# Performance work log

Measured on AMD Instinct MI355X. Metric: run time of the kernel, lower is better.

The kernel has to match this reference:

```python
import jax, jax.numpy as jnp
import numpy as np

N_NODES = 30000
N_EDGES = 240000
N_GRAPHS = 300
IN_CH = 5


def _bn(x, p):
    # inference batchnorm; p = stack([gamma, beta, running_mean, running_var]), shape (4, C)
    g, b, m, v = p
    return g * (x - m) * jax.lax.rsqrt(v + 1e-5) + b


def _gatv2(x, src, dst, wl, bl, wr, br, att, bias, heads, outc, concat):
    # PyG GATv2Conv: e_ij = att . leaky_relu(lin_l(x_j) + lin_r(x_i)), softmax over edges into i,
    # out_i = sum_j alpha_ij * lin_l(x_j)
    n = x.shape[0]
    xl = (x @ wl + bl).reshape(n, heads, outc)  # source-side transform
    xr = (x @ wr + br).reshape(n, heads, outc)  # target-side transform
    e = jax.nn.leaky_relu(xl[src] + xr[dst], 0.2)          # [E, H, C]
    logit = jnp.einsum('ehc,hc->eh', e, att)               # [E, H]
    lmax = jax.ops.segment_max(logit, dst, num_segments=n)
    lmax = jnp.where(jnp.isfinite(lmax), lmax, 0.0)        # empty segments -> 0
    ex = jnp.exp(logit - lmax[dst])
    den = jax.ops.segment_sum(ex, dst, num_segments=n)
    alpha = ex / (den[dst] + 1e-16)                        # PyG softmax eps
    out = jax.ops.segment_sum(xl[src] * alpha[..., None], dst, num_segments=n)
    out = out.reshape(n, heads * outc) if concat else out.mean(axis=1)
    return out + bias


def _forward(x, edge_index, batch, w_in, b_in, bn_in,
             g1_wl, g1_bl, g1_wr, g1_br, g1_att, g1_bias, bn1,
             g2_wl, g2_bl, g2_wr, g2_br, g2_att, g2_bias, bn2,
             g3_wl, g3_bl, g3_wr, g3_br, g3_att, g3_bias, bn3,
             c_w1, c_b1, c_bn, c_w2, c_b2, c_w3, c_b3):
    n = x.shape[0]
    loops = jnp.arange(n)
    src = jnp.concatenate([edge_index[0], loops])  # add_self_loops=True
    dst = jnp.concatenate([edge_index[1], loops])
    h = jax.nn.relu(_bn(x @ w_in + b_in, bn_in))
    h = jax.nn.elu(_bn(_gatv2(h, src, dst, g1_wl, g1_bl, g1_wr, g1_br, g1_att, g1_bias, 4, 64, True), bn1))
    h = jax.nn.elu(_bn(_gatv2(h, src, dst, g2_wl, g2_bl, g2_wr, g2_br, g2_att, g2_bias, 4, 64, True), bn2))
    h = jax.nn.elu(_bn(_gatv2(h, src, dst, g3_wl, g3_bl, g3_wr, g3_br, g3_att, g3_bias, 1, 128, False), bn3))
    cnt = jax.ops.segment_sum(jnp.ones((n,), h.dtype), batch, num_segments=N_GRAPHS)
    mean = jax.ops.segment_sum(h, batch, num_segments=N_GRAPHS) / jnp.maximum(cnt, 1.0)[:, None]
    mx = jax.ops.segment_max(h, batch, num_segments=N_GRAPHS)
    mx = jnp.where(jnp.isfinite(mx), mx, 0.0)
    g = jnp.concatenate([mean, mx], axis=1)                # (B, 256)
    z = jax.nn.relu(_bn(g @ c_w1 + c_b1, c_bn))
    z = jax.nn.relu(z @ c_w2 + c_b2)
    return jax.nn.log_softmax(z @ c_w3 + c_b3, axis=-1)    # (B, 2)


def setup_inputs() -> dict:
    base = jax.random.key(0)
    k = lambda i: jax.random.fold_in(base, i)
    def lin(i, fi, fo):
        return jax.random.normal(k(i), (fi, fo), jnp.float32) / np.sqrt(np.float32(fi))
    def vec(i, c):
        return jax.random.normal(k(i), (c,), jnp.float32) * 0.05
    def bn(i, c):
        g = jax.random.uniform(k(i), (c,), jnp.float32) + 0.5
        b = jax.random.normal(jax.random.fold_in(k(i), 1), (c,), jnp.float32) * 0.1
        return jnp.stack([g, b, jnp.zeros((c,), jnp.float32), jnp.ones((c,), jnp.float32)])
    def att(i, h, c):
        return jax.random.normal(k(i), (h, c), jnp.float32) / np.sqrt(np.float32(c))
    return dict(
        x=jax.random.normal(k(0), (N_NODES, IN_CH), jnp.float32),
        edge_index=jax.random.randint(k(1), (2, N_EDGES), 0, N_NODES),
        batch=jnp.sort(jax.random.randint(k(2), (N_NODES,), 0, N_GRAPHS)),
        w_in=lin(3, IN_CH, 64), b_in=vec(4, 64), bn_in=bn(5, 64),
        g1_wl=lin(6, 64, 256), g1_bl=vec(7, 256), g1_wr=lin(8, 64, 256), g1_br=vec(9, 256),
        g1_att=att(10, 4, 64), g1_bias=vec(11, 256), bn1=bn(12, 256),
        g2_wl=lin(13, 256, 256), g2_bl=vec(14, 256), g2_wr=lin(15, 256, 256), g2_br=vec(16, 256),
        g2_att=att(17, 4, 64), g2_bias=vec(18, 256), bn2=bn(19, 256),
        g3_wl=lin(20, 256, 128), g3_bl=vec(21, 128), g3_wr=lin(22, 256, 128), g3_br=vec(23, 128),
        g3_att=att(24, 1, 128), g3_bias=vec(25, 128), bn3=bn(26, 128),
        c_w1=lin(27, 256, 128), c_b1=vec(28, 128), c_bn=bn(29, 128),
        c_w2=lin(30, 128, 64), c_b2=vec(31, 64),
        c_w3=lin(32, 64, 2), c_b3=vec(33, 2),
    )


def reference(x, edge_index, batch, w_in, b_in, bn_in,
              g1_wl, g1_bl, g1_wr, g1_br, g1_att, g1_bias, bn1,
              g2_wl, g2_bl, g2_wr, g2_br, g2_att, g2_bias, bn2,
              g3_wl, g3_bl, g3_wr, g3_br, g3_att, g3_bias, bn3,
              c_w1, c_b1, c_bn, c_w2, c_b2, c_w3, c_b3):
    return _forward(x, edge_index, batch, w_in, b_in, bn_in,
                    g1_wl, g1_bl, g1_wr, g1_br, g1_att, g1_bias, bn1,
                    g2_wl, g2_bl, g2_wr, g2_br, g2_att, g2_bias, bn2,
                    g3_wl, g3_bl, g3_wr, g3_br, g3_att, g3_bias, bn3,
                    c_w1, c_b1, c_bn, c_w2, c_b2, c_w3, c_b3)
```

## Files before the change

### kernel.cpp

```cpp
#include <hip/hip_runtime.h>
#include <math.h>

#define N_NODES  30000
#define N_EDGES  240000
#define E_TOT    270000
#define N_GRAPHS 300
#define NCH      118

typedef _Float16 half8 __attribute__((ext_vector_type(8)));
typedef _Float16 half4 __attribute__((ext_vector_type(4)));
typedef _Float16 half2v __attribute__((ext_vector_type(2)));
typedef float float4v __attribute__((ext_vector_type(4)));

static inline int cdiv(int a, int b) { return (a + b - 1) / b; }

__device__ inline void wp_dev(const float* __restrict__ W, _Float16* __restrict__ Wt,
                              int K, int CO, int gtid, int T) {
    int tot = K * CO;
    for (int i = gtid; i < tot; i += T) {
        int k = i / CO, c = i - k * CO;
        Wt[(size_t)c * K + k] = (_Float16)W[i];
    }
}

__global__ void hist_wprep_input(const int* __restrict__ ei, int* __restrict__ deg,
                                 const float* __restrict__ x, const float* __restrict__ w_in,
                                 const float* __restrict__ b_in, const float* __restrict__ bn_in,
                                 _Float16* __restrict__ a16,
                                 const float* __restrict__ w1l, const float* __restrict__ w1r,
                                 const float* __restrict__ w2l, const float* __restrict__ w2r,
                                 const float* __restrict__ w3l, const float* __restrict__ w3r,
                                 _Float16* __restrict__ t1l, _Float16* __restrict__ t1r,
                                 _Float16* __restrict__ t2l, _Float16* __restrict__ t2r,
                                 _Float16* __restrict__ t3l, _Float16* __restrict__ t3r) {
    int gtid = blockIdx.x * blockDim.x + threadIdx.x;
    int T = gridDim.x * blockDim.x;
    for (int e = gtid; e < E_TOT; e += T) {
        int d = (e < N_EDGES) ? ei[N_EDGES + e] : e - N_EDGES;
        atomicAdd(&deg[d], 1);
    }
    wp_dev(w1l, t1l, 64, 256, gtid, T);
    wp_dev(w1r, t1r, 64, 256, gtid, T);
    wp_dev(w2l, t2l, 256, 256, gtid, T);
    wp_dev(w2r, t2r, 256, 256, gtid, T);
    wp_dev(w3l, t3l, 256, 128, gtid, T);
    wp_dev(w3r, t3r, 256, 128, gtid, T);

    int lane = threadIdx.x & 63;
    int wv = blockIdx.x * (blockDim.x >> 6) + (threadIdx.x >> 6);
    int NW = gridDim.x * (blockDim.x >> 6);
    float g = bn_in[lane], be = bn_in[64 + lane];
    float m = bn_in[128 + lane], va = bn_in[192 + lane];
    float rs = rsqrtf(va + 1e-5f);
    float wcol[5];
#pragma unroll
    for (int ci = 0; ci < 5; ++ci) wcol[ci] = w_in[ci * 64 + lane];
    float bb = b_in[lane];
    for (int n = wv; n < N_NODES; n += NW) {
        float xv = (lane < 5) ? x[n * 5 + lane] : 0.f;
        float acc = bb;
#pragma unroll
        for (int ci = 0; ci < 5; ++ci)
            acc = fmaf(__shfl(xv, ci, 64), wcol[ci], acc);
        acc = g * (acc - m) * rs + be;
        a16[(size_t)n * 64 + lane] = (_Float16)fmaxf(acc, 0.f);
    }
}

__global__ __launch_bounds__(256)
void scan_all(const int* __restrict__ deg, const int* __restrict__ batch,
              int* __restrict__ row_start, int* __restrict__ gstart) {
    __shared__ int red[256];
    __shared__ int s[256];
    const int b = blockIdx.x, t = threadIdx.x;
    int pre = 0;
    for (int i = t; i < b * 256; i += 256) pre += deg[i];
    red[t] = pre;
    __syncthreads();
    for (int off = 128; off; off >>= 1) {
        if (t < off) red[t] += red[t + off];
        __syncthreads();
    }
    int base = red[0];
    int gid = b * 256 + t;
    int v = (gid < N_NODES) ? deg[gid] : 0;
    s[t] = v;
    __syncthreads();
    for (int off = 1; off < 256; off <<= 1) {
        int u = (t >= off) ? s[t - off] : 0;
        __syncthreads();
        s[t] += u;
        __syncthreads();
    }
    if (gid < N_NODES) row_start[gid] = base + s[t] - v;
    if (b == 0 && t == 0) row_start[N_NODES] = E_TOT;
    if (b == 0) {
        for (int g = t; g <= N_GRAPHS; g += 256) {
            int lo = 0, hi = N_NODES;
            while (lo < hi) {
                int mid = (lo + hi) >> 1;
                if (batch[mid] < g) lo = mid + 1;
                else                hi = mid;
            }
            gstart[g] = lo;
        }
    }
}

template<int K, int COUT, int SCAT>
__global__ __launch_bounds__(256, 3)
void gemm_mfma(const _Float16* __restrict__ A,
               const _Float16* __restrict__ Wtl, const float* __restrict__ bl,
               const _Float16* __restrict__ Wtr, const float* __restrict__ br,
               _Float16* __restrict__ outl, _Float16* __restrict__ outr,
               const int* __restrict__ ei, const int* __restrict__ row_start,
               int* __restrict__ cnt, int* __restrict__ esrc, int N) {
    constexpr int BM = 128, BN = 128, BK = 64;
    constexpr int LDK = BK + 8;
    constexpr int CSL = COUT / BN > 0 ? COUT / BN : 1;
    if (SCAT && blockIdx.y == 2 * CSL) {
        int gtid = blockIdx.x * blockDim.x + threadIdx.x;
        int T = gridDim.x * blockDim.x;
        for (int e = gtid; e < E_TOT; e += T) {
            int s, d;
            if (e < N_EDGES) { s = ei[e]; d = ei[N_EDGES + e]; }
            else             { s = e - N_EDGES; d = s; }
            int slot = row_start[d] + atomicAdd(&cnt[d], 1);
            esrc[slot] = s;
        }
        return;
    }
    __shared__ _Float16 As[BM][LDK];
    __shared__ _Float16 Bs[BN][LDK];
    const int tid  = threadIdx.x;
    const int wave = tid >> 6;
    const int lane = tid & 63;
    const int l15  = lane & 15;
    const int lq   = lane >> 4;
    const int n0   = blockIdx.x * BM;
    const int sel  = blockIdx.y / CSL;
    const int col0 = (blockIdx.y % CSL) * BN;
    const _Float16* Wt = sel ? Wtr : Wtl;
    const float* bias  = sel ? br : bl;
    _Float16* out      = sel ? outr : outl;

    float4v acc[2][8];
#pragma unroll
    for (int mi = 0; mi < 2; ++mi)
#pragma unroll
        for (int nt = 0; nt < 8; ++nt)
#pragma unroll
            for (int r = 0; r < 4; ++r) acc[mi][nt][r] = 0.f;

    for (int kt = 0; kt < K; kt += BK) {
#pragma unroll
        for (int p = 0; p < 4; ++p) {
            int idx = p * 256 + tid;
            int row = idx >> 3;
            int ch  = (idx & 7) * 8;
            int gn  = n0 + row;
            half8 v = {};
            if (gn < N) v = *(const half8*)(A + (size_t)gn * K + kt + ch);
            *(half8*)(&As[row][ch]) = v;
        }
#pragma unroll
        for (int p = 0; p < 4; ++p) {
            int idx = p * 256 + tid;
            int row = idx >> 3;
            int ch  = (idx & 7) * 8;
            half8 v = *(const half8*)(Wt + (size_t)(col0 + row) * K + kt + ch);
            *(half8*)(&Bs[row][ch]) = v;
        }
        __syncthreads();
#pragma unroll
        for (int kk = 0; kk < BK; kk += 32) {
            half8 af0 = *(const half8*)(&As[wave * 32 + l15][kk + lq * 8]);
            half8 af1 = *(const half8*)(&As[wave * 32 + 16 + l15][kk + lq * 8]);
#pragma unroll
            for (int nt = 0; nt < 8; ++nt) {
                half8 bf = *(const half8*)(&Bs[nt * 16 + l15][kk + lq * 8]);
                acc[0][nt] = __builtin_amdgcn_mfma_f32_16x16x32_f16(af0, bf, acc[0][nt], 0, 0, 0);
                acc[1][nt] = __builtin_amdgcn_mfma_f32_16x16x32_f16(af1, bf, acc[1][nt], 0, 0, 0);
            }
        }
        __syncthreads();
    }
#pragma unroll
    for (int mi = 0; mi < 2; ++mi)
#pragma unroll
        for (int nt = 0; nt < 8; ++nt) {
            int col = col0 + nt * 16 + l15;
            float bv = bias[col];
#pragma unroll
            for (int r = 0; r < 4; ++r) {
                int row = n0 + wave * 32 + mi * 16 + lq * 4 + r;
                if (row < N)
                    out[(size_t)row * COUT + col] = (_Float16)(acc[mi][nt][r] + bv);
            }
        }
}

template<typename TOUT>
__global__ __launch_bounds__(256)
void gat_gather4(const _Float16* __restrict__ xl, const _Float16* __restrict__ xr,
                 const int* __restrict__ row_start, const int* __restrict__ esrc,
                 const float* __restrict__ att, const float* __restrict__ gbias,
                 const float* __restrict__ bnp, TOUT* __restrict__ out) {
    constexpr int HC = 256, PER = 4, GROUP = 16;
    int node = (blockIdx.x * blockDim.x + threadIdx.x) >> 6;
    int lane = threadIdx.x & 63;
    if (node >= N_NODES) return;
    const int base = lane * PER;

    float rr[PER], av[PER], acc[PER];
    {
        half4 rv = *(const half4*)(xr + (size_t)node * HC + base);
#pragma unroll
        for (int k = 0; k < PER; ++k) rr[k] = (float)rv[k];
        *(float4*)av = *(const float4*)(att + base);
    }
#pragma unroll
    for (int k = 0; k < PER; ++k) acc[k] = 0.f;

    float l = 0.f;
    const int j0 = row_start[node], j1 = row_start[node + 1];
    for (int jc = j0; jc < j1; jc += 64) {
        int nedge = min(64, j1 - jc);
        int ev = (jc + lane < j1) ? esrc[jc + lane] : 0;
        for (int jj = 0; jj < nedge; jj += 4) {
            int s[4];
            bool val[4];
#pragma unroll
            for (int u = 0; u < 4; ++u) {
                int idx = jj + u;
                val[u] = idx < nedge;
                s[u] = __shfl(ev, val[u] ? idx : jj, 64);
            }
            float xs[4][PER];
#pragma unroll
            for (int u = 0; u < 4; ++u) {
                half4 xv = *(const half4*)(xl + (size_t)s[u] * HC + base);
#pragma unroll
                for (int k = 0; k < PER; ++k) xs[u][k] = (float)xv[k];
            }
            float pz[4];
#pragma unroll
            for (int u = 0; u < 4; ++u) {
                float pp = 0.f;
#pragma unroll
                for (int k = 0; k < PER; ++k) {
                    float v = xs[u][k] + rr[k];
                    v = (v > 0.f) ? v : 0.2f * v;
                    pp = fmaf(v, av[k], pp);
                }
                pz[u] = pp;
            }
#pragma unroll
            for (int off = GROUP / 2; off; off >>= 1) {
#pragma unroll
                for (int u = 0; u < 4; ++u) pz[u] += __shfl_xor(pz[u], off, 64);
            }
            float w[4];
#pragma unroll
            for (int u = 0; u < 4; ++u) w[u] = val[u] ? __expf(pz[u]) : 0.f;
            l += (w[0] + w[1]) + (w[2] + w[3]);
#pragma unroll
            for (int k = 0; k < PER; ++k)
                acc[k] += fmaf(w[0], xs[0][k],
                          fmaf(w[1], xs[1][k],
                          fmaf(w[2], xs[2][k], w[3] * xs[3][k])));
        }
    }
    float inv = 1.f / (l + 1e-16f);
    float o[PER];
#pragma unroll
    for (int k = 0; k < PER; ++k) {
        float v = fmaf(acc[k], inv, gbias[base + k]);
        float g  = bnp[base + k], be = bnp[HC + base + k];
        float mm = bnp[2 * HC + base + k], va = bnp[3 * HC + base + k];
        v = g * (v - mm) * rsqrtf(va + 1e-5f) + be;
        o[k] = (v > 0.f) ? v : (__expf(v) - 1.f);
    }
    half4 ov;
#pragma unroll
    for (int k = 0; k < PER; ++k) ov[k] = (_Float16)o[k];
    *(half4*)((_Float16*)out + (size_t)node * HC + base) = ov;
}

__global__ __launch_bounds__(256)
void gat_gather1(const _Float16* __restrict__ xl, const _Float16* __restrict__ xr,
                 const int* __restrict__ row_start, const int* __restrict__ esrc,
                 const float* __restrict__ att, const float* __restrict__ gbias,
                 const float* __restrict__ bnp, float* __restrict__ out) {
    constexpr int HC = 128, PER = 4;
    int node = (blockIdx.x * blockDim.x + threadIdx.x) >> 6;
    int lane = threadIdx.x & 63;
    if (node >= N_NODES) return;
    const int half = lane >> 5;
    const int base = (lane & 31) * PER;

    float rr[PER], av[PER], acc[PER];
    {
        half4 rv = *(const half4*)(xr + (size_t)node * HC + base);
#pragma unroll
        for (int k = 0; k < PER; ++k) rr[k] = (float)rv[k];
        *(float4*)av = *(const float4*)(att + base);
    }
#pragma unroll
    for (int k = 0; k < PER; ++k) acc[k] = 0.f;

    float l = 0.f;
    const int j0 = row_start[node], j1 = row_start[node + 1];
    for (int jc = j0; jc < j1; jc += 64) {
        int nedge = min(64, j1 - jc);
        int ev = (jc + lane < j1) ? esrc[jc + lane] : 0;
        for (int jj = 0; jj < nedge; jj += 8) {
            int s[4];
            bool val[4];
#pragma unroll
            for (int u = 0; u < 4; ++u) {
                int idx = jj + 2 * u + half;
                val[u] = idx < nedge;
                s[u] = __shfl(ev, val[u] ? idx : jj, 64);
            }
            float xs[4][PER];
#pragma unroll
            for (int u = 0; u < 4; ++u) {
                half4 xv = *(const half4*)(xl + (size_t)s[u] * HC + base);
#pragma unroll
                for (int k = 0; k < PER; ++k) xs[u][k] = (float)xv[k];
            }
            float pz[4];
#pragma unroll
            for (int u = 0; u < 4; ++u) {
                float pp = 0.f;
#pragma unroll
                for (int k = 0; k < PER; ++k) {
                    float v = xs[u][k] + rr[k];
                    v = (v > 0.f) ? v : 0.2f * v;
                    pp = fmaf(v, av[k], pp);
                }
                pz[u] = pp;
            }
#pragma unroll
            for (int off = 16; off; off >>= 1) {
#pragma unroll
                for (int u = 0; u < 4; ++u) pz[u] += __shfl_xor(pz[u], off, 64);
            }
            float w[4];
#pragma unroll
            for (int u = 0; u < 4; ++u) w[u] = val[u] ? __expf(pz[u]) : 0.f;
            l += (w[0] + w[1]) + (w[2] + w[3]);
#pragma unroll
            for (int k = 0; k < PER; ++k)
                acc[k] += fmaf(w[0], xs[0][k],
                          fmaf(w[1], xs[1][k],
                          fmaf(w[2], xs[2][k], w[3] * xs[3][k])));
        }
    }
    l += __shfl_xor(l, 32, 64);
#pragma unroll
    for (int k = 0; k < PER; ++k) acc[k] += __shfl_xor(acc[k], 32, 64);

    if (half == 0) {
        float inv = 1.f / (l + 1e-16f);
        float o[PER];
#pragma unroll
        for (int k = 0; k < PER; ++k) {
            float v = fmaf(acc[k], inv, gbias[base + k]);
            float g  = bnp[base + k], be = bnp[HC + base + k];
            float mm = bnp[2 * HC + base + k], va = bnp[3 * HC + base + k];
            v = g * (v - mm) * rsqrtf(va + 1e-5f) + be;
            o[k] = (v > 0.f) ? v : (__expf(v) - 1.f);
        }
        *(float4*)(out + (size_t)node * HC + base) = *(float4*)o;
    }
}

__global__ void pool_cls(const float* __restrict__ h, const int* __restrict__ gstart,
                         const float* __restrict__ w1, const float* __restrict__ b1,
                         const float* __restrict__ bnp,
                         const float* __restrict__ w2, const float* __restrict__ b2,
                         const float* __restrict__ w3, const float* __restrict__ b3,
                         float* __restrict__ out) {
    __shared__ float sg[256];
    __shared__ float sz1[128];
    __shared__ float sz2[64];
    __shared__ float sz3[2];
    int g = blockIdx.x, t = threadIdx.x;
    int a = gstart[g], b = gstart[g + 1];
    float sum = 0.f, mx = -INFINITY;
    for (int i = a; i < b; ++i) {
        float v = h[(size_t)i * 128 + t];
        sum += v;
        mx = fmaxf(mx, v);
    }
    sg[t]       = sum / fmaxf((float)(b - a), 1.f);
    sg[128 + t] = (b > a) ? mx : 0.f;
    __syncthreads();
    float acc = b1[t];
    for (int i = 0; i < 256; ++i) acc += sg[i] * w1[i * 128 + t];
    float ga = bnp[t], be = bnp[128 + t], m = bnp[256 + t], va = bnp[384 + t];
    acc = ga * (acc - m) * rsqrtf(va + 1e-5f) + be;
    sz1[t] = fmaxf(acc, 0.f);
    __syncthreads();
    if (t < 64) {
        float a2 = b2[t];
        for (int i = 0; i < 128; ++i) a2 += sz1[i] * w2[i * 64 + t];
        sz2[t] = fmaxf(a2, 0.f);
    }
    __syncthreads();
    if (t < 2) {
        float a3 = b3[t];
        for (int i = 0; i < 64; ++i) a3 += sz2[i] * w3[i * 2 + t];
        sz3[t] = a3;
    }
    __syncthreads();
    if (t < 2) {
        float mm = fmaxf(sz3[0], sz3[1]);
        float lse = mm + logf(expf(sz3[0] - mm) + expf(sz3[1] - mm));
        out[g * 2 + t] = sz3[t] - lse;
    }
}

extern "C" void kernel_launch(void* const* d_in, const int* in_sizes, int n_in,
                              void* d_out, int out_size, void* d_ws, size_t ws_size,
                              hipStream_t stream) {
    const float* x       = (const float*)d_in[0];
    const int*   ei      = (const int*)d_in[1];
    const int*   batch   = (const int*)d_in[2];
    const float* w_in    = (const float*)d_in[3];
    const float* b_in    = (const float*)d_in[4];
    const float* bn_in   = (const float*)d_in[5];
    const float* g1_wl   = (const float*)d_in[6];
    const float* g1_bl   = (const float*)d_in[7];
    const float* g1_wr   = (const float*)d_in[8];
    const float* g1_br   = (const float*)d_in[9];
    const float* g1_att  = (const float*)d_in[10];
    const float* g1_bias = (const float*)d_in[11];
    const float* bn1     = (const float*)d_in[12];
    const float* g2_wl   = (const float*)d_in[13];
    const float* g2_bl   = (const float*)d_in[14];
    const float* g2_wr   = (const float*)d_in[15];
    const float* g2_br   = (const float*)d_in[16];
    const float* g2_att  = (const float*)d_in[17];
    const float* g2_bias = (const float*)d_in[18];
    const float* bn2     = (const float*)d_in[19];
    const float* g3_wl   = (const float*)d_in[20];
    const float* g3_bl   = (const float*)d_in[21];
    const float* g3_wr   = (const float*)d_in[22];
    const float* g3_br   = (const float*)d_in[23];
    const float* g3_att  = (const float*)d_in[24];
    const float* g3_bias = (const float*)d_in[25];
    const float* bn3     = (const float*)d_in[26];
    const float* c_w1    = (const float*)d_in[27];
    const float* c_b1    = (const float*)d_in[28];
    const float* c_bn    = (const float*)d_in[29];
    const float* c_w2    = (const float*)d_in[30];
    const float* c_b2    = (const float*)d_in[31];
    const float* c_w3    = (const float*)d_in[32];
    const float* c_b3    = (const float*)d_in[33];
    float* out = (float*)d_out;

    const size_t NHC = (size_t)N_NODES * 256;
    _Float16* a16  = (_Float16*)d_ws;
    _Float16* xl16 = a16 + NHC;
    _Float16* xr16 = xl16 + NHC;
    _Float16* wt = xr16 + NHC;
    _Float16* wt1l = wt;            _Float16* wt1r = wt + 16384;
    _Float16* wt2l = wt + 32768;    _Float16* wt2r = wt + 98304;
    _Float16* wt3l = wt + 163840;   _Float16* wt3r = wt + 196608;
    float* fbase = (float*)(wt + 262144);
    float* bufD = fbase;
    int* iw = (int*)(bufD + (size_t)N_NODES * 128);
    int* deg       = iw;            int* cnt    = iw + 30000;
    int* row_start = iw + 90128;
    int* esrc      = iw + 120129;
    int* gstart    = iw + 390429;

    const int BT = 256;
    const int NT128 = cdiv(N_NODES, 128);

    hipMemsetAsync(deg, 0, 60000 * sizeof(int), stream);

    hist_wprep_input<<<1024, BT, 0, stream>>>(ei, deg, x, w_in, b_in, bn_in, a16,
                                              g1_wl, g1_wr, g2_wl, g2_wr, g3_wl, g3_wr,
                                              wt1l, wt1r, wt2l, wt2r, wt3l, wt3r);
    scan_all<<<NCH, 256, 0, stream>>>(deg, batch, row_start, gstart);

    gemm_mfma<64, 256, 1><<<dim3(NT128, 5), 256, 0, stream>>>(
        a16, wt1l, g1_bl, wt1r, g1_br, xl16, xr16, ei, row_start, cnt, esrc, N_NODES);
    gat_gather4<_Float16><<<cdiv(N_NODES * 64, BT), BT, 0, stream>>>(
        xl16, xr16, row_start, esrc, g1_att, g1_bias, bn1, a16);

    gemm_mfma<256, 256, 0><<<dim3(NT128, 4), 256, 0, stream>>>(
        a16, wt2l, g2_bl, wt2r, g2_br, xl16, xr16, nullptr, nullptr, nullptr, nullptr, N_NODES);
    gat_gather4<_Float16><<<cdiv(N_NODES * 64, BT), BT, 0, stream>>>(
        xl16, xr16, row_start, esrc, g2_att, g2_bias, bn2, a16);

    gemm_mfma<256, 128, 0><<<dim3(NT128, 2), 256, 0, stream>>>(
        a16, wt3l, g3_bl, wt3r, g3_br, xl16, xr16, nullptr, nullptr, nullptr, nullptr, N_NODES);
    gat_gather1<<<cdiv(N_NODES * 64, BT), BT, 0, stream>>>(
        xl16, xr16, row_start, esrc, g3_att, g3_bias, bn3, bufD);

    pool_cls<<<N_GRAPHS, 128, 0, stream>>>(bufD, gstart, c_w1, c_b1, c_bn,
                                           c_w2, c_b2, c_w3, c_b3, out);
}
```

Baseline: 374.1 us.

## Use direct global-to-LDS loads with XOR swizzle, DPP reductions, wider pooling

The GEMM tile loads now go straight from global memory into LDS through global_load_lds, replacing the register-staged copies. An XOR swizzle on the LDS layout stands in for the old padding, and occupancy is raised to 4 blocks. In the gather kernels the 16-lane shuffle-xor reductions become DPP row-rotate adds, and the pooling/classifier kernel spreads its node loop and matvecs over 512 threads with partial-sum reductions. Out-of-range rows are clamped to row 0 rather than zero-filled, which is safe only because those rows are never stored.

```diff
diff --git a/kernel.cpp b/kernel.cpp
--- a/kernel.cpp
+++ b/kernel.cpp
@@ -13,6 +13,25 @@
 typedef float float4v __attribute__((ext_vector_type(4)));
 
 static inline int cdiv(int a, int b) { return (a + b - 1) / b; }
+
+static __device__ __forceinline__ void gload_lds16(const void* g, void* l) {
+    __builtin_amdgcn_global_load_lds(
+        (const __attribute__((address_space(1))) void*)g,
+        (__attribute__((address_space(3))) void*)l, 16, 0, 0);
+}
+
+template<int CTRL>
+static __device__ __forceinline__ float ror_add(float v) {
+    int t = __builtin_amdgcn_update_dpp(0, __float_as_int(v), CTRL, 0xF, 0xF, false);
+    return v + __int_as_float(t);
+}
+static __device__ __forceinline__ float red16(float v) {
+    v = ror_add<0x128>(v);
+    v = ror_add<0x124>(v);
+    v = ror_add<0x122>(v);
+    v = ror_add<0x121>(v);
+    return v;
+}
 
 __device__ inline void wp_dev(const float* __restrict__ W, _Float16* __restrict__ Wt,
                               int K, int CO, int gtid, int T) {
@@ -108,7 +127,7 @@
 }
 
 template<int K, int COUT, int SCAT>
-__global__ __launch_bounds__(256, 3)
+__global__ __launch_bounds__(256, 4)
 void gemm_mfma(const _Float16* __restrict__ A,
                const _Float16* __restrict__ Wtl, const float* __restrict__ bl,
                const _Float16* __restrict__ Wtr, const float* __restrict__ br,
@@ -116,7 +135,6 @@
                const int* __restrict__ ei, const int* __restrict__ row_start,
                int* __restrict__ cnt, int* __restrict__ esrc, int N) {
     constexpr int BM = 128, BN = 128, BK = 64;
-    constexpr int LDK = BK + 8;
     constexpr int CSL = COUT / BN > 0 ? COUT / BN : 1;
     if (SCAT && blockIdx.y == 2 * CSL) {
         int gtid = blockIdx.x * blockDim.x + threadIdx.x;
@@ -130,8 +148,8 @@
         }
         return;
     }
-    __shared__ _Float16 As[BM][LDK];
-    __shared__ _Float16 Bs[BN][LDK];
+    __shared__ __attribute__((aligned(16))) _Float16 As[BM * BK];
+    __shared__ __attribute__((aligned(16))) _Float16 Bs[BN * BK];
     const int tid  = threadIdx.x;
     const int wave = tid >> 6;
     const int lane = tid & 63;
@@ -144,6 +162,9 @@
     const float* bias  = sel ? br : bl;
     _Float16* out      = sel ? outr : outl;
 
+    const int r0 = tid >> 3;
+    const int us = (tid & 7) ^ (r0 & 7);
+
     float4v acc[2][8];
 #pragma unroll
     for (int mi = 0; mi < 2; ++mi)
@@ -155,30 +176,25 @@
     for (int kt = 0; kt < K; kt += BK) {
 #pragma unroll
         for (int p = 0; p < 4; ++p) {
-            int idx = p * 256 + tid;
-            int row = idx >> 3;
-            int ch  = (idx & 7) * 8;
+            int row = p * 32 + r0;
             int gn  = n0 + row;
-            half8 v = {};
-            if (gn < N) v = *(const half8*)(A + (size_t)gn * K + kt + ch);
-            *(half8*)(&As[row][ch]) = v;
+            if (gn >= N) gn = 0;
+            gload_lds16(A + (size_t)gn * K + kt + us * 8, As + (p * 256 + tid) * 8);
         }
 #pragma unroll
         for (int p = 0; p < 4; ++p) {
-            int idx = p * 256 + tid;
-            int row = idx >> 3;
-            int ch  = (idx & 7) * 8;
-            half8 v = *(const half8*)(Wt + (size_t)(col0 + row) * K + kt + ch);
-            *(half8*)(&Bs[row][ch]) = v;
+            int row = p * 32 + r0;
+            gload_lds16(Wt + (size_t)(col0 + row) * K + kt + us * 8, Bs + (p * 256 + tid) * 8);
         }
         __syncthreads();
 #pragma unroll
         for (int kk = 0; kk < BK; kk += 32) {
-            half8 af0 = *(const half8*)(&As[wave * 32 + l15][kk + lq * 8]);
-            half8 af1 = *(const half8*)(&As[wave * 32 + 16 + l15][kk + lq * 8]);
+            const int sw = (lq + (kk >> 3)) ^ (l15 & 7);
+            half8 af0 = *(const half8*)(As + (wave * 32 + l15) * BK + sw * 8);
+            half8 af1 = *(const half8*)(As + (wave * 32 + 16 + l15) * BK + sw * 8);
 #pragma unroll
             for (int nt = 0; nt < 8; ++nt) {
-                half8 bf = *(const half8*)(&Bs[nt * 16 + l15][kk + lq * 8]);
+                half8 bf = *(const half8*)(Bs + (nt * 16 + l15) * BK + sw * 8);
                 acc[0][nt] = __builtin_amdgcn_mfma_f32_16x16x32_f16(af0, bf, acc[0][nt], 0, 0, 0);
                 acc[1][nt] = __builtin_amdgcn_mfma_f32_16x16x32_f16(af1, bf, acc[1][nt], 0, 0, 0);
             }
@@ -206,7 +222,7 @@
                  const int* __restrict__ row_start, const int* __restrict__ esrc,
                  const float* __restrict__ att, const float* __restrict__ gbias,
                  const float* __restrict__ bnp, TOUT* __restrict__ out) {
-    constexpr int HC = 256, PER = 4, GROUP = 16;
+    constexpr int HC = 256, PER = 4;
     int node = (blockIdx.x * blockDim.x + threadIdx.x) >> 6;
     int lane = threadIdx.x & 63;
     if (node >= N_NODES) return;
@@ -253,12 +269,7 @@
                     v = (v > 0.f) ? v : 0.2f * v;
                     pp = fmaf(v, av[k], pp);
                 }
-                pz[u] = pp;
-            }
-#pragma unroll
-            for (int off = GROUP / 2; off; off >>= 1) {
-#pragma unroll
-                for (int u = 0; u < 4; ++u) pz[u] += __shfl_xor(pz[u], off, 64);
+                pz[u] = red16(pp);
             }
             float w[4];
 #pragma unroll
@@ -340,12 +351,8 @@
                     v = (v > 0.f) ? v : 0.2f * v;
                     pp = fmaf(v, av[k], pp);
                 }
-                pz[u] = pp;
-            }
-#pragma unroll
-            for (int off = 16; off; off >>= 1) {
-#pragma unroll
-                for (int u = 0; u < 4; ++u) pz[u] += __shfl_xor(pz[u], off, 64);
+                pp += __shfl_xor(pp, 16, 64);
+                pz[u] = red16(pp);
             }
             float w[4];
 #pragma unroll
@@ -377,38 +384,60 @@
     }
 }
 
-__global__ void pool_cls(const float* __restrict__ h, const int* __restrict__ gstart,
-                         const float* __restrict__ w1, const float* __restrict__ b1,
-                         const float* __restrict__ bnp,
-                         const float* __restrict__ w2, const float* __restrict__ b2,
-                         const float* __restrict__ w3, const float* __restrict__ b3,
-                         float* __restrict__ out) {
+__global__ __launch_bounds__(512)
+void pool_cls(const float* __restrict__ h, const int* __restrict__ gstart,
+              const float* __restrict__ w1, const float* __restrict__ b1,
+              const float* __restrict__ bnp,
+              const float* __restrict__ w2, const float* __restrict__ b2,
+              const float* __restrict__ w3, const float* __restrict__ b3,
+              float* __restrict__ out) {
+    __shared__ float part[512];
     __shared__ float sg[256];
     __shared__ float sz1[128];
     __shared__ float sz2[64];
     __shared__ float sz3[2];
     int g = blockIdx.x, t = threadIdx.x;
+    int c = t & 127, q = t >> 7;
     int a = gstart[g], b = gstart[g + 1];
     float sum = 0.f, mx = -INFINITY;
-    for (int i = a; i < b; ++i) {
-        float v = h[(size_t)i * 128 + t];
+    for (int i = a + q; i < b; i += 4) {
+        float v = h[(size_t)i * 128 + c];
         sum += v;
         mx = fmaxf(mx, v);
     }
-    sg[t]       = sum / fmaxf((float)(b - a), 1.f);
-    sg[128 + t] = (b > a) ? mx : 0.f;
-    __syncthreads();
-    float acc = b1[t];
-    for (int i = 0; i < 256; ++i) acc += sg[i] * w1[i * 128 + t];
-    float ga = bnp[t], be = bnp[128 + t], m = bnp[256 + t], va = bnp[384 + t];
-    acc = ga * (acc - m) * rsqrtf(va + 1e-5f) + be;
-    sz1[t] = fmaxf(acc, 0.f);
-    __syncthreads();
-    if (t < 64) {
-        float a2 = b2[t];
-        for (int i = 0; i < 128; ++i) a2 += sz1[i] * w2[i * 64 + t];
-        sz2[t] = fmaxf(a2, 0.f);
-    }
+    part[t] = sum;
+    __syncthreads();
+    if (q == 0)
+        sg[c] = (part[c] + part[c + 128] + part[c + 256] + part[c + 384])
+                / fmaxf((float)(b - a), 1.f);
+    __syncthreads();
+    part[t] = mx;
+    __syncthreads();
+    if (q == 0) {
+        float m2 = fmaxf(fmaxf(part[c], part[c + 128]),
+                         fmaxf(part[c + 256], part[c + 384]));
+        sg[128 + c] = (b > a) ? m2 : 0.f;
+    }
+    __syncthreads();
+    float acc = 0.f;
+    for (int i = q * 64; i < q * 64 + 64; ++i) acc += sg[i] * w1[i * 128 + c];
+    part[t] = acc;
+    __syncthreads();
+    if (q == 0) {
+        float z = part[c] + part[c + 128] + part[c + 256] + part[c + 384] + b1[c];
+        float ga = bnp[c], be = bnp[128 + c], m = bnp[256 + c], va = bnp[384 + c];
+        z = ga * (z - m) * rsqrtf(va + 1e-5f) + be;
+        sz1[c] = fmaxf(z, 0.f);
+    }
+    __syncthreads();
+    if (t < 128) {
+        int o = t & 63, q2 = t >> 6;
+        float a2 = 0.f;
+        for (int i = q2 * 64; i < q2 * 64 + 64; ++i) a2 += sz1[i] * w2[i * 64 + o];
+        part[t] = a2;
+    }
+    __syncthreads();
+    if (t < 64) sz2[t] = fmaxf(part[t] + part[t + 64] + b2[t], 0.f);
     __syncthreads();
     if (t < 2) {
         float a3 = b3[t];
@@ -503,6 +532,6 @@
     gat_gather1<<<cdiv(N_NODES * 64, BT), BT, 0, stream>>>(
         xl16, xr16, row_start, esrc, g3_att, g3_bias, bn3, bufD);
 
-    pool_cls<<<N_GRAPHS, 128, 0, stream>>>(bufD, gstart, c_w1, c_b1, c_bn,
+    pool_cls<<<N_GRAPHS, 512, 0, stream>>>(bufD, gstart, c_w1, c_b1, c_bn,
                                            c_w2, c_b2, c_w3, c_b3, out);
 }
```

Result: faster. 315.6 us (-15.6%).
